# Kernel optimization log

Hardware: AMD Instinct MI355X
Metric: run time of the kernel (lower is better)

The kernel has to match this reference:

```python
import jax, jax.numpy as jnp
import numpy as np


def _ctc_greedy_decode(probs, table, default_char):
    """Greedy CTC decode (tf.keras.backend.ctc_decode, greedy=True) + label->char lookup.

    probs: [B, T, C] post-softmax scores; blank index = C-1 (tf convention).
    Returns [B, T] int32 char codes, left-packed, padded positions -> default_char
    (tf pads the dense decoded tensor with -1; the hash-table lookup of -1 yields
    the table's default value).
    """
    B, T, C = probs.shape
    blank = C - 1
    best = jnp.argmax(probs, axis=-1).astype(jnp.int32)           # [B, T]
    # collapse repeats: keep first of each run
    prev = jnp.concatenate([jnp.full((B, 1), -1, jnp.int32), best[:, :-1]], axis=1)
    valid = (best != prev) & (best != blank)                      # [B, T]
    # left-pack valid labels via scatter (invalid entries routed to a dummy column T)
    pos = jnp.cumsum(valid.astype(jnp.int32), axis=1) - 1         # output slot per step
    scatter_col = jnp.where(valid, pos, T)
    out = jnp.full((B, T + 1), -1, jnp.int32)
    b_idx = jnp.arange(B)[:, None]
    out = out.at[b_idx, scatter_col].set(best)
    labels = out[:, :T]                                           # [B, T], -1 padded
    # hash-table lookup: valid labels -> chars, -1 padding -> default_value
    chars = jnp.where(labels >= 0,
                      table[jnp.clip(labels, 0, C - 1)],
                      jnp.int32(default_char))
    return chars


def setup_inputs() -> dict:
    key = jax.random.key(0)
    k1, k2 = jax.random.split(key)
    B, T, C = 1024, 512, 128
    inputs = jax.random.uniform(k1, (B, T, C), dtype=jnp.float32)
    table = jax.random.randint(k2, (C,), 0, 128, dtype=jnp.int32)
    return {"inputs": inputs, "table": table, "default_char": 32}


def reference(inputs, table, default_char):
    return _ctc_greedy_decode(inputs, table, default_char)
```

## Files before the change

kernel.cpp:

```cpp
#include <hip/hip_runtime.h>


constexpr int T_DIM = 512;
constexpr int C_DIM = 128;
constexpr int BLANK = C_DIM - 1;
constexpr int BLOCK = 512;

__global__ __launch_bounds__(BLOCK) void ctc_decode_kernel(
    const float* __restrict__ probs,
    const int* __restrict__ table,
    const int* __restrict__ defc_p,
    int* __restrict__ out)
{
    __shared__ int s_best[T_DIM];
    __shared__ int s_chars[T_DIM];
    __shared__ int s_table[C_DIM];
    __shared__ int s_wavesums[BLOCK / 64];

    const int b    = blockIdx.x;
    const int tid  = threadIdx.x;
    const int lane = tid & 63;
    const int wave = tid >> 6;

    if (tid < C_DIM) s_table[tid] = table[tid];
    const int defc = defc_p[0];

    const float* row = probs + (size_t)b * T_DIM * C_DIM;

    const int half = lane >> 5;
    const int s    = lane & 31;
    for (int it = 0; it < T_DIM / 16; ++it) {
        const int t = it * 16 + wave * 2 + half;
        const float4 v4 = *(const float4*)(row + (size_t)t * C_DIM + s * 4);
        float bv = v4.x; int bi = s * 4;
        if (v4.y > bv) { bv = v4.y; bi = s * 4 + 1; }
        if (v4.z > bv) { bv = v4.z; bi = s * 4 + 2; }
        if (v4.w > bv) { bv = v4.w; bi = s * 4 + 3; }
        #pragma unroll
        for (int m = 16; m >= 1; m >>= 1) {
            const float ov = __shfl_xor(bv, m);
            const int   oi = __shfl_xor(bi, m);
            if (ov > bv || (ov == bv && oi < bi)) { bv = ov; bi = oi; }
        }
        if (s == 0) s_best[t] = bi;
    }
    __syncthreads();

    const int best_t = s_best[tid];
    const int prev   = (tid > 0) ? s_best[tid - 1] : -1;
    const int valid  = (best_t != prev && best_t != BLANK) ? 1 : 0;

    int scan = valid;
    #pragma unroll
    for (int off = 1; off < 64; off <<= 1) {
        const int v = __shfl_up(scan, off);
        if (lane >= off) scan += v;
    }
    if (lane == 63) s_wavesums[wave] = scan;
    __syncthreads();
    if (tid == 0) {
        int acc = 0;
        #pragma unroll
        for (int w = 0; w < BLOCK / 64; ++w) {
            const int tmp = s_wavesums[w];
            s_wavesums[w] = acc;
            acc += tmp;
        }
    }
    __syncthreads();
    const int pos = scan + s_wavesums[wave] - 1;

    s_chars[tid] = defc;
    __syncthreads();
    if (valid) s_chars[pos] = s_table[best_t];
    __syncthreads();
    out[(size_t)b * T_DIM + tid] = s_chars[tid];
}

extern "C" void kernel_launch(void* const* d_in, const int* in_sizes, int n_in,
                              void* d_out, int out_size, void* d_ws, size_t ws_size,
                              hipStream_t stream) {
    const float* probs = (const float*)d_in[0];
    const int*   table = (const int*)d_in[1];
    const int*   defc  = (const int*)d_in[2];
    int*         out   = (int*)d_out;

    const int B = out_size / T_DIM;
    ctc_decode_kernel<<<dim3(B), dim3(BLOCK), 0, stream>>>(probs, table, defc, out);
}
```

Baseline: 362.4 us.

## Stage probability tiles through LDS with register prefetch for argmax

Replaces per-row wave-level shuffle argmax with a tiled scheme. Each 128-timestep tile is loaded into registers, written to padded shared memory, and the next tile is prefetched while four threads per timestep scan 32 classes each and combine with two shuffle steps. The goal is to overlap global loads with compute and cut shuffle work. In exchange it uses about 66KB of LDS per block, which can limit occupancy. It also starts the argmax at -1.0, which assumes non-negative inputs.

```diff
diff --git a/kernel.cpp b/kernel.cpp
--- a/kernel.cpp
+++ b/kernel.cpp
@@ -1,17 +1,22 @@
 #include <hip/hip_runtime.h>
 
 
-constexpr int T_DIM = 512;
-constexpr int C_DIM = 128;
-constexpr int BLANK = C_DIM - 1;
-constexpr int BLOCK = 512;
+constexpr int T_DIM   = 512;
+constexpr int C_DIM   = 128;
+constexpr int BLANK   = C_DIM - 1;
+constexpr int BLOCK   = 512;
+constexpr int TILE_T  = 128;
+constexpr int N_TILES = T_DIM / TILE_T;
+constexpr int ROW_W   = 132;
+constexpr int LDS_TILE_WORDS = TILE_T * ROW_W;
 
-__global__ __launch_bounds__(BLOCK) void ctc_decode_kernel(
+__global__ __launch_bounds__(BLOCK, 4) void ctc_decode_kernel(
     const float* __restrict__ probs,
     const int* __restrict__ table,
     const int* __restrict__ defc_p,
     int* __restrict__ out)
 {
+    __shared__ float s_tile[LDS_TILE_WORDS];
     __shared__ int s_best[T_DIM];
     __shared__ int s_chars[T_DIM];
     __shared__ int s_table[C_DIM];
@@ -27,22 +32,51 @@
 
     const float* row = probs + (size_t)b * T_DIM * C_DIM;
 
-    const int half = lane >> 5;
-    const int s    = lane & 31;
-    for (int it = 0; it < T_DIM / 16; ++it) {
-        const int t = it * 16 + wave * 2 + half;
-        const float4 v4 = *(const float4*)(row + (size_t)t * C_DIM + s * 4);
-        float bv = v4.x; int bi = s * 4;
-        if (v4.y > bv) { bv = v4.y; bi = s * 4 + 1; }
-        if (v4.z > bv) { bv = v4.z; bi = s * 4 + 2; }
-        if (v4.w > bv) { bv = v4.w; bi = s * 4 + 3; }
+    const int ts = tid >> 2;
+    const int q  = tid & 3;
+
+    float4 pf[8];
+    {
+        const float4* src = (const float4*)row;
         #pragma unroll
-        for (int m = 16; m >= 1; m >>= 1) {
+        for (int j = 0; j < 8; ++j) pf[j] = src[j * BLOCK + tid];
+    }
+
+    for (int tile = 0; tile < N_TILES; ++tile) {
+        __syncthreads();
+        #pragma unroll
+        for (int j = 0; j < 8; ++j) {
+            const int idx4 = j * BLOCK + tid;
+            const int wts  = idx4 >> 5;
+            const int m    = idx4 & 31;
+            *(float4*)&s_tile[wts * ROW_W + m * 4] = pf[j];
+        }
+        __syncthreads();
+
+        if (tile + 1 < N_TILES) {
+            const float4* src = (const float4*)(row + (size_t)(tile + 1) * TILE_T * C_DIM);
+            #pragma unroll
+            for (int j = 0; j < 8; ++j) pf[j] = src[j * BLOCK + tid];
+        }
+
+        const float* base = &s_tile[ts * ROW_W + q * 32];
+        float bv = -1.0f; int bi = 0;
+        #pragma unroll
+        for (int k = 0; k < 8; ++k) {
+            const float4 v = *(const float4*)(base + 4 * k);
+            const int i0 = q * 32 + 4 * k;
+            if (v.x > bv) { bv = v.x; bi = i0;     }
+            if (v.y > bv) { bv = v.y; bi = i0 + 1; }
+            if (v.z > bv) { bv = v.z; bi = i0 + 2; }
+            if (v.w > bv) { bv = v.w; bi = i0 + 3; }
+        }
+        #pragma unroll
+        for (int m = 1; m <= 2; m <<= 1) {
             const float ov = __shfl_xor(bv, m);
             const int   oi = __shfl_xor(bi, m);
             if (ov > bv || (ov == bv && oi < bi)) { bv = ov; bi = oi; }
         }
-        if (s == 0) s_best[t] = bi;
+        if (q == 0) s_best[tile * TILE_T + ts] = bi;
     }
     __syncthreads();
 
```

New measurement: 390.4 us. +7.7%, slower.

## Restructure argmax: 8 lanes per row, register prefetch, packed-key shuffle reduction

Applied to the files above, without the earlier changes.

Each row is now handled by 8 lanes that each load four float4 chunks, so a wave covers 8 timesteps per iteration instead of 2. The next iteration's loads are prefetched into registers while the current one is reduced. The cross-lane argmax packs value bits and the inverted index into one 64-bit key and reduces it with 3 shuffle steps instead of 5 paired shuffles. The aim is more memory-level parallelism and fewer shuffle instructions, at the cost of more registers per thread. The -1 initial value and unsigned float comparison are correct only for non-negative inputs such as softmax outputs.

```diff
diff --git a/kernel.cpp b/kernel.cpp
--- a/kernel.cpp
+++ b/kernel.cpp
@@ -5,8 +5,10 @@
 constexpr int C_DIM = 128;
 constexpr int BLANK = C_DIM - 1;
 constexpr int BLOCK = 512;
+constexpr int TS_PER_ITER = BLOCK / 8;
+constexpr int N_ITER = T_DIM / TS_PER_ITER;
 
-__global__ __launch_bounds__(BLOCK) void ctc_decode_kernel(
+__global__ __launch_bounds__(BLOCK, 4) void ctc_decode_kernel(
     const float* __restrict__ probs,
     const int* __restrict__ table,
     const int* __restrict__ defc_p,
@@ -27,22 +29,47 @@
 
     const float* row = probs + (size_t)b * T_DIM * C_DIM;
 
-    const int half = lane >> 5;
-    const int s    = lane & 31;
-    for (int it = 0; it < T_DIM / 16; ++it) {
-        const int t = it * 16 + wave * 2 + half;
-        const float4 v4 = *(const float4*)(row + (size_t)t * C_DIM + s * 4);
-        float bv = v4.x; int bi = s * 4;
-        if (v4.y > bv) { bv = v4.y; bi = s * 4 + 1; }
-        if (v4.z > bv) { bv = v4.z; bi = s * 4 + 2; }
-        if (v4.w > bv) { bv = v4.w; bi = s * 4 + 3; }
+    const int g = lane >> 3;
+    const int h = lane & 7;
+
+    float4 pf[4];
+    {
+        const float* p0 = row + (size_t)(wave * 8 + g) * C_DIM + h * 4;
         #pragma unroll
-        for (int m = 16; m >= 1; m >>= 1) {
-            const float ov = __shfl_xor(bv, m);
-            const int   oi = __shfl_xor(bi, m);
-            if (ov > bv || (ov == bv && oi < bi)) { bv = ov; bi = oi; }
+        for (int j = 0; j < 4; ++j) pf[j] = *(const float4*)(p0 + j * 32);
+    }
+
+    for (int it = 0; it < N_ITER; ++it) {
+        float4 v[4];
+        #pragma unroll
+        for (int j = 0; j < 4; ++j) v[j] = pf[j];
+
+        if (it + 1 < N_ITER) {
+            const float* pn = row + (size_t)((it + 1) * TS_PER_ITER + wave * 8 + g) * C_DIM + h * 4;
+            #pragma unroll
+            for (int j = 0; j < 4; ++j) pf[j] = *(const float4*)(pn + j * 32);
         }
-        if (s == 0) s_best[t] = bi;
+
+        float bv = -1.0f; int bi = 0;
+        #pragma unroll
+        for (int j = 0; j < 4; ++j) {
+            const int i0 = j * 32 + h * 4;
+            if (v[j].x > bv) { bv = v[j].x; bi = i0;     }
+            if (v[j].y > bv) { bv = v[j].y; bi = i0 + 1; }
+            if (v[j].z > bv) { bv = v[j].z; bi = i0 + 2; }
+            if (v[j].w > bv) { bv = v[j].w; bi = i0 + 3; }
+        }
+
+        unsigned long long key =
+            ((unsigned long long)__float_as_uint(bv) << 32) | (unsigned)(127 - bi);
+
+        #pragma unroll
+        for (int m = 1; m <= 4; m <<= 1) {
+            const unsigned long long ok = __shfl_xor(key, m);
+            if (ok > key) key = ok;
+        }
+
+        if (h == 0) s_best[it * TS_PER_ITER + wave * 8 + g] = 127 - (int)(key & 127u);
     }
     __syncthreads();
 
@@ -53,8 +80,8 @@
     int scan = valid;
     #pragma unroll
     for (int off = 1; off < 64; off <<= 1) {
-        const int v = __shfl_up(scan, off);
-        if (lane >= off) scan += v;
+        const int vv = __shfl_up(scan, off);
+        if (lane >= off) scan += vv;
     }
     if (lane == 63) s_wavesums[wave] = scan;
     __syncthreads();
```

Result: no change. 355.7 us (-1.9%).
